# Kernel optimization log

Measured on AMD Instinct MI355X. Metric: run time of the kernel, lower is better.

## Reference

```python
import jax, jax.numpy as jnp
import numpy as np

N_NODES = 100000
N_EDGES = 1600000
IN_CH = 128
HEADS = 4
HID = 32
OUT_CH = 128
NEG_SLOPE = 0.2


def setup_inputs() -> dict:
    key = jax.random.key(0)
    ks = jax.random.split(key, 7)
    sc = 1.0 / np.sqrt(IN_CH)
    return {
        "x": jax.random.normal(ks[0], (N_NODES, IN_CH), dtype=jnp.float32),
        "edge_index": jax.random.randint(ks[1], (2, N_EDGES), 0, N_NODES, dtype=jnp.int32),
        "W": jax.random.normal(ks[2], (IN_CH, HEADS * HID), dtype=jnp.float32) * sc,
        "att_src": jax.random.normal(ks[3], (HEADS, HID), dtype=jnp.float32) * sc,
        "att_dst": jax.random.normal(ks[4], (HEADS, HID), dtype=jnp.float32) * sc,
        "lin_w": jax.random.normal(ks[5], (HEADS * HID, OUT_CH), dtype=jnp.float32) * (1.0 / np.sqrt(HEADS * HID)),
        "lin_b": jax.random.normal(ks[6], (OUT_CH,), dtype=jnp.float32) * 0.01,
    }


def reference(x, edge_index, W, att_src, att_dst, lin_w, lin_b):
    N = x.shape[0]
    src, dst = edge_index[0], edge_index[1]
    # node-wise linear transform -> [N, H, C]
    h = (x @ W).reshape(N, HEADS, HID)
    # per-node attention logit components [N, H]
    a_src = jnp.einsum("nhc,hc->nh", h, att_src)
    a_dst = jnp.einsum("nhc,hc->nh", h, att_dst)
    # per-edge logits with LeakyReLU [E, H]
    e = jax.nn.leaky_relu(a_src[src] + a_dst[dst], negative_slope=NEG_SLOPE)
    # segment softmax over destination neighborhoods
    m = jax.ops.segment_max(e, dst, num_segments=N)
    ex = jnp.exp(e - m[dst])
    s = jax.ops.segment_sum(ex, dst, num_segments=N)
    alpha = ex / (s[dst] + 1e-16)
    # weighted scatter-sum of source features [N, H, C] -> concat heads
    msg = h[src] * alpha[:, :, None]
    out = jax.ops.segment_sum(msg, dst, num_segments=N).reshape(N, HEADS * HID)
    # trailing dense + ReLU
    return jax.nn.relu(out @ lin_w + lin_b)
```

## Files before the change

### kernel.cpp

```cpp
#include <hip/hip_runtime.h>
#include <hip/hip_fp16.h>

#define NB   256
#define NBLK 128
#define BSH  9
#define DB   64
#define DBLK 128

typedef _Float16 f16;
typedef _Float16 half8 __attribute__((ext_vector_type(8)));
typedef __fp16 pk16x2 __attribute__((ext_vector_type(2)));
typedef float f32x4 __attribute__((ext_vector_type(4)));

__global__ void k_prep(const float* __restrict__ W, const float* __restrict__ LW,
                       f16* __restrict__ Wt, f16* __restrict__ LWt)
{
    int n = blockIdx.x & 127;
    const float* src = (blockIdx.x < 128) ? W : LW;
    f16* dst = (blockIdx.x < 128) ? Wt : LWt;
    int k = threadIdx.x;
    dst[n * 128 + k] = (f16)src[k * 128 + n];
}

__global__ __launch_bounds__(256) void k_gemm_att(
    const float* __restrict__ A, const f16* __restrict__ Wt,
    const float* __restrict__ att_s, const float* __restrict__ att_d,
    f16* __restrict__ Hh, float* __restrict__ as_out, float* __restrict__ ad_out,
    int M)
{
    __shared__ __align__(16) f16 as_lds[64 * 136];
    int t = threadIdx.x;
    int row0 = blockIdx.x * 64;

    {
        int r = t >> 2, kq = (t & 3) * 32;
        const float* ap = A + (size_t)(row0 + r) * 128 + kq;
        bool valid = (row0 + r) < M;
        pk16x2 hb[16];
#pragma unroll
        for (int j = 0; j < 8; ++j) {
            float4 v = valid ? *(const float4*)(ap + j * 4) : make_float4(0.f, 0.f, 0.f, 0.f);
            hb[2 * j]     = __builtin_amdgcn_cvt_pkrtz(v.x, v.y);
            hb[2 * j + 1] = __builtin_amdgcn_cvt_pkrtz(v.z, v.w);
        }
        f16* dst = as_lds + r * 136 + kq;
#pragma unroll
        for (int j = 0; j < 4; ++j) *(float4*)(dst + j * 8) = ((float4*)hb)[j];
    }
    __syncthreads();

    int w = t >> 6, ln = t & 63;
    int rr = (w & 1) * 32;
    int cc = (w >> 1) * 64;
    int q = ln >> 4, m = ln & 15;

    f32x4 acc[2][4];
#pragma unroll
    for (int i = 0; i < 2; ++i)
#pragma unroll
        for (int j = 0; j < 4; ++j) acc[i][j] = (f32x4){0.f, 0.f, 0.f, 0.f};

    const f16* wp = Wt + (size_t)(cc + m) * 128 + q * 8;
#pragma unroll
    for (int ks = 0; ks < 4; ++ks) {
        int k0 = ks * 32 + q * 8;
        half8 a0 = *(const half8*)(as_lds + (rr + m) * 136 + k0);
        half8 a1 = *(const half8*)(as_lds + (rr + 16 + m) * 136 + k0);
        half8 bf[4];
#pragma unroll
        for (int j = 0; j < 4; ++j)
            bf[j] = *(const half8*)(wp + j * 16 * 128 + ks * 32);
#pragma unroll
        for (int j = 0; j < 4; ++j) {
            acc[0][j] = __builtin_amdgcn_mfma_f32_16x16x32_f16(a0, bf[j], acc[0][j], 0, 0, 0);
            acc[1][j] = __builtin_amdgcn_mfma_f32_16x16x32_f16(a1, bf[j], acc[1][j], 0, 0, 0);
        }
    }
    __syncthreads();
#pragma unroll
    for (int i = 0; i < 2; ++i)
#pragma unroll
        for (int j = 0; j < 4; ++j)
#pragma unroll
            for (int g = 0; g < 4; ++g)
                as_lds[(rr + i * 16 + q * 4 + g) * 136 + cc + j * 16 + m] = (f16)acc[i][j][g];
    __syncthreads();
    {
        int r = t >> 2, cq = (t & 3) * 32;
        if (row0 + r < M) {
            float4 o0 = *(const float4*)(as_lds + r * 136 + cq);
            float4 o1 = *(const float4*)(as_lds + r * 136 + cq + 8);
            float4 o2 = *(const float4*)(as_lds + r * 136 + cq + 16);
            float4 o3 = *(const float4*)(as_lds + r * 136 + cq + 24);
            float4* hp = (float4*)(Hh + (size_t)(row0 + r) * 128 + cq);
            hp[0] = o0; hp[1] = o1; hp[2] = o2; hp[3] = o3;
        }
    }
    {
        int rl = w * 16 + m;
        int head = q;
        float ds = 0.f, dd = 0.f;
#pragma unroll
        for (int ch = 0; ch < 4; ++ch) {
            half8 hv = *(const half8*)(as_lds + rl * 136 + head * 32 + ch * 8);
            float4 s0 = *(const float4*)(att_s + head * 32 + ch * 8);
            float4 s1 = *(const float4*)(att_s + head * 32 + ch * 8 + 4);
            float4 d0 = *(const float4*)(att_d + head * 32 + ch * 8);
            float4 d1 = *(const float4*)(att_d + head * 32 + ch * 8 + 4);
            ds += (float)hv[0] * s0.x + (float)hv[1] * s0.y + (float)hv[2] * s0.z + (float)hv[3] * s0.w
                + (float)hv[4] * s1.x + (float)hv[5] * s1.y + (float)hv[6] * s1.z + (float)hv[7] * s1.w;
            dd += (float)hv[0] * d0.x + (float)hv[1] * d0.y + (float)hv[2] * d0.z + (float)hv[3] * d0.w
                + (float)hv[4] * d1.x + (float)hv[5] * d1.y + (float)hv[6] * d1.z + (float)hv[7] * d1.w;
        }
        if (row0 + rl < M) {
            as_out[(row0 + rl) * 4 + head] = ds;
            ad_out[(row0 + rl) * 4 + head] = dd;
        }
    }
}


__global__ __launch_bounds__(256) void k_ph_hist(
    const int* __restrict__ dst, int* __restrict__ bh, int E, int chunk)
{
    __shared__ int hist[NB];
    int t = threadIdx.x;
    hist[t] = 0;
    __syncthreads();
    int e0 = blockIdx.x * chunk;
    int e1 = min(e0 + chunk, E);
    for (int e = e0 + t; e < e1; e += 256)
        atomicAdd(&hist[dst[e] >> BSH], 1);
    __syncthreads();
    bh[t * NBLK + blockIdx.x] = hist[t];
}

__global__ __launch_bounds__(1024) void k_ph_scan(int* __restrict__ bh)
{
    __shared__ int sd[1024];
    const int per = (NB * NBLK) / 1024;
    int t = threadIdx.x;
    int base = t * per;
    int loc[per];
    int sum = 0;
#pragma unroll
    for (int j = 0; j < per; ++j) { loc[j] = bh[base + j]; sum += loc[j]; }
    sd[t] = sum;
    __syncthreads();
    for (int o = 1; o < 1024; o <<= 1) {
        int x = (t >= o) ? sd[t - o] : 0;
        __syncthreads();
        sd[t] += x;
        __syncthreads();
    }
    int run = sd[t] - sum;
#pragma unroll
    for (int j = 0; j < per; ++j) { bh[base + j] = run; run += loc[j]; }
}

__global__ __launch_bounds__(256) void k_ph_bin(
    const int* __restrict__ ei, const int* __restrict__ bh,
    int* __restrict__ binned, int E, int chunk)
{
    __shared__ int boff[NB];
    int t = threadIdx.x;
    boff[t] = bh[t * NBLK + blockIdx.x];
    __syncthreads();
    int e0 = blockIdx.x * chunk;
    int e1 = min(e0 + chunk, E);
    for (int e = e0 + t; e < e1; e += 256) {
        int s = ei[e];
        int d = ei[E + e];
        int p = atomicAdd(&boff[d >> BSH], 1);
        binned[p] = s | ((d & ((1 << BSH) - 1)) << 17);
    }
}

__global__ __launch_bounds__(256) void k_ph_csr(
    const int* __restrict__ binned, const int* __restrict__ bh,
    int* __restrict__ csr, int* __restrict__ off, int* __restrict__ deg,
    int N, int E)
{
    __shared__ int cnt[512], loff[512], sd[256];
    int b = blockIdx.x;
    int lo = b << BSH;
    if (lo >= N) return;
    int t = threadIdx.x;
    int seg = bh[b * NBLK];
    int segend = (b + 1 < NB) ? bh[(b + 1) * NBLK] : E;
    int len = segend - seg;
    cnt[t] = 0; cnt[t + 256] = 0;
    __syncthreads();
    for (int i = t; i < len; i += 256)
        atomicAdd(&cnt[(unsigned)binned[seg + i] >> 17], 1);
    __syncthreads();
    int a0 = cnt[2 * t], a1 = cnt[2 * t + 1];
    int s = a0 + a1;
    sd[t] = s;
    __syncthreads();
    for (int o = 1; o < 256; o <<= 1) {
        int x = (t >= o) ? sd[t - o] : 0;
        __syncthreads();
        sd[t] += x;
        __syncthreads();
    }
    int ex = sd[t] - s;
    loff[2 * t] = ex;
    loff[2 * t + 1] = ex + a0;
    int n0 = lo + 2 * t;
    if (n0 < N)     { off[n0] = seg + ex;          deg[n0] = a0; }
    if (n0 + 1 < N) { off[n0 + 1] = seg + ex + a0; deg[n0 + 1] = a1; }
    __syncthreads();
    for (int i = t; i < len; i += 256) {
        int v = binned[seg + i];
        int p = atomicAdd(&loff[(unsigned)v >> 17], 1);
        csr[seg + p] = v & 0x1ffff;
    }
}

__global__ __launch_bounds__(256) void k_dhist(
    const int* __restrict__ deg, int* __restrict__ dh, int N, int chunk)
{
    __shared__ int h[DB];
    int t = threadIdx.x;
    if (t < DB) h[t] = 0;
    __syncthreads();
    int e0 = blockIdx.x * chunk;
    int e1 = min(e0 + chunk, N);
    for (int i = e0 + t; i < e1; i += 256)
        atomicAdd(&h[min(deg[i], DB - 1)], 1);
    __syncthreads();
    if (t < DB) dh[t * DBLK + blockIdx.x] = h[t];
}

__global__ __launch_bounds__(1024) void k_dscan(int* __restrict__ dh)
{
    __shared__ int sd[1024];
    const int per = (DB * DBLK) / 1024;
    int t = threadIdx.x;
    int base = t * per;
    int loc[per];
    int sum = 0;
#pragma unroll
    for (int j = 0; j < per; ++j) { loc[j] = dh[base + j]; sum += loc[j]; }
    sd[t] = sum;
    __syncthreads();
    for (int o = 1; o < 1024; o <<= 1) {
        int x = (t >= o) ? sd[t - o] : 0;
        __syncthreads();
        sd[t] += x;
        __syncthreads();
    }
    int run = sd[t] - sum;
#pragma unroll
    for (int j = 0; j < per; ++j) { dh[base + j] = run; run += loc[j]; }
}

__global__ __launch_bounds__(256) void k_dscat(
    const int* __restrict__ deg, const int* __restrict__ dh,
    int* __restrict__ perm, int N, int chunk)
{
    __shared__ int boff[DB];
    int t = threadIdx.x;
    if (t < DB) boff[t] = dh[t * DBLK + blockIdx.x];
    __syncthreads();
    int e0 = blockIdx.x * chunk;
    int e1 = min(e0 + chunk, N);
    for (int i = e0 + t; i < e1; i += 256) {
        int p = atomicAdd(&boff[min(deg[i], DB - 1)], 1);
        perm[p] = i;
    }
}

__global__ __launch_bounds__(256) void k_gather_fused(
    const __half* __restrict__ Hh, const float* __restrict__ as_,
    const float* __restrict__ ad_, const int* __restrict__ off,
    const int* __restrict__ deg, const int* __restrict__ csr,
    const int* __restrict__ perm, const f16* __restrict__ LWt,
    const float* __restrict__ bias, float* __restrict__ Out, int N)
{
    __shared__ __align__(16) __half2 wh[16][68];
    __shared__ int srcs[16][16];
    __shared__ __align__(16) f16 pt[16][136];
    __shared__ int pnode[16];
    int t = threadIdx.x;
    int wid = t >> 6, lane = t & 63;
    int sub = lane >> 4;
    int li = lane & 15;
    int hh = li >> 2;
    int slot = wid * 4 + sub;
    int gbase = blockIdx.x * 16;
    if (t < 16) pnode[t] = (gbase + t < N) ? perm[gbase + t] : -1;
    __syncthreads();
    int n = pnode[slot];
    bool nvalid = n >= 0;
    int dg = nvalid ? deg[n] : 0;
    int base = nvalid ? off[n] : 0;
    float4 adn = nvalid ? *(const float4*)(ad_ + (size_t)n * 4)
                        : make_float4(0.f, 0.f, 0.f, 0.f);

    float s0 = 0.f, s1 = 0.f, s2 = 0.f, s3 = 0.f;
    float acc[8] = {0.f, 0.f, 0.f, 0.f, 0.f, 0.f, 0.f, 0.f};

    for (int c0 = 0; c0 < dg; c0 += 16) {
        int cnt = min(16, dg - c0);
        {
            int idx = c0 + li;
            int se = csr[base + min(idx, dg - 1)];
            float4 as = *(const float4*)(as_ + (size_t)se * 4);
            float e0 = as.x + adn.x, e1 = as.y + adn.y;
            float e2 = as.z + adn.z, e3 = as.w + adn.w;
            e0 = fmaxf(e0, 0.2f * e0); e1 = fmaxf(e1, 0.2f * e1);
            e2 = fmaxf(e2, 0.2f * e2); e3 = fmaxf(e3, 0.2f * e3);
            float x0 = __expf(e0), x1 = __expf(e1);
            float x2 = __expf(e2), x3 = __expf(e3);
            if (idx >= dg) { x0 = x1 = x2 = x3 = 0.f; }
            s0 += x0; s1 += x1; s2 += x2; s3 += x3;
            __half2 w4[4];
            w4[0] = __float2half2_rn(x0);
            w4[1] = __float2half2_rn(x1);
            w4[2] = __float2half2_rn(x2);
            w4[3] = __float2half2_rn(x3);
            *(float4*)&wh[slot][li * 4] = *(float4*)w4;
            srcs[slot][li] = se;
        }
        __asm__ volatile("s_waitcnt lgkmcnt(0)" ::: "memory");
        int quads = (cnt + 3) >> 2;
        __half2 ah[4];
        ah[0] = ah[1] = ah[2] = ah[3] = __float2half2_rn(0.f);
        for (int qq = 0; qq < quads; ++qq) {
#pragma unroll
            for (int u = 0; u < 4; ++u) {
                int i = qq * 4 + u;
                __half2 w2 = wh[slot][i * 4 + hh];
                int se = srcs[slot][i];
                float4 raw = *(const float4*)(Hh + (size_t)se * 128 + li * 8);
                __half2* ph = (__half2*)&raw;
                ah[0] = __hfma2(ph[0], w2, ah[0]);
                ah[1] = __hfma2(ph[1], w2, ah[1]);
                ah[2] = __hfma2(ph[2], w2, ah[2]);
                ah[3] = __hfma2(ph[3], w2, ah[3]);
            }
            if ((qq & 1) == 1) {
#pragma unroll
                for (int k = 0; k < 4; ++k) {
                    float2 f = __half22float2(ah[k]);
                    acc[2 * k] += f.x; acc[2 * k + 1] += f.y;
                    ah[k] = __float2half2_rn(0.f);
                }
            }
        }
#pragma unroll
        for (int k = 0; k < 4; ++k) {
            float2 f = __half22float2(ah[k]);
            acc[2 * k] += f.x; acc[2 * k + 1] += f.y;
        }
        __asm__ volatile("s_waitcnt lgkmcnt(0)" ::: "memory");
    }

#pragma unroll
    for (int o = 1; o < 16; o <<= 1) {
        s0 += __shfl_xor(s0, o);
        s1 += __shfl_xor(s1, o);
        s2 += __shfl_xor(s2, o);
        s3 += __shfl_xor(s3, o);
    }
    float sh = (hh == 0) ? s0 : (hh == 1) ? s1 : (hh == 2) ? s2 : s3;
    float inv = 1.f / (sh + 1e-16f);
    {
        __half2 o4[4];
#pragma unroll
        for (int k = 0; k < 4; ++k)
            o4[k] = __float22half2_rn(make_float2(acc[2 * k] * inv, acc[2 * k + 1] * inv));
        *(float4*)&pt[slot][li * 8] = *(float4*)o4;
    }
    __syncthreads();

    {
        int cc = wid * 32;
        f32x4 acc2[2];
        acc2[0] = (f32x4){0.f, 0.f, 0.f, 0.f};
        acc2[1] = (f32x4){0.f, 0.f, 0.f, 0.f};
        const f16* wp = LWt + (size_t)(cc + li) * 128 + sub * 8;
#pragma unroll
        for (int ks = 0; ks < 4; ++ks) {
            half8 a0 = *(const half8*)&pt[li][ks * 32 + sub * 8];
            half8 b0 = *(const half8*)(wp + ks * 32);
            half8 b1 = *(const half8*)(wp + 16 * 128 + ks * 32);
            acc2[0] = __builtin_amdgcn_mfma_f32_16x16x32_f16(a0, b0, acc2[0], 0, 0, 0);
            acc2[1] = __builtin_amdgcn_mfma_f32_16x16x32_f16(a0, b1, acc2[1], 0, 0, 0);
        }
        float bv0 = bias[cc + li];
        float bv1 = bias[cc + 16 + li];
#pragma unroll
        for (int g = 0; g < 4; ++g) {
            int r = sub * 4 + g;
            int node = pnode[r];
            if (node >= 0) {
                Out[(size_t)node * 128 + cc + li]      = fmaxf(acc2[0][g] + bv0, 0.f);
                Out[(size_t)node * 128 + cc + 16 + li] = fmaxf(acc2[1][g] + bv1, 0.f);
            }
        }
    }
}


extern "C" void kernel_launch(void* const* d_in, const int* in_sizes, int n_in,
                              void* d_out, int out_size, void* d_ws, size_t ws_size,
                              hipStream_t stream)
{
    const float* x     = (const float*)d_in[0];
    const int*   ei    = (const int*)d_in[1];
    const float* W     = (const float*)d_in[2];
    const float* att_s = (const float*)d_in[3];
    const float* att_d = (const float*)d_in[4];
    const float* lin_w = (const float*)d_in[5];
    const float* lin_b = (const float*)d_in[6];
    float* out = (float*)d_out;
    int N = in_sizes[0] / 128;
    int E = in_sizes[1] / 2;

    char* p = (char*)d_ws;
    auto alloc = [&](size_t bytes) { char* r = p; p += (bytes + 255) & ~(size_t)255; return r; };
    f16*    Hh   = (f16*)alloc((size_t)N * 128 * 2);
    f16*    Wt   = (f16*)alloc(128 * 128 * 2);
    f16*    LWt  = (f16*)alloc(128 * 128 * 2);
    float*  AS   = (float*)alloc((size_t)N * 4 * 4);
    float*  AD   = (float*)alloc((size_t)N * 4 * 4);
    int*    deg  = (int*)alloc((size_t)N * 4);
    int*    off  = (int*)alloc((size_t)N * 4);
    int*    perm = (int*)alloc((size_t)N * 4);
    int*    csr  = (int*)alloc((size_t)E * 4);
    int*    binned = (int*)alloc((size_t)E * 4);
    int*    bh   = (int*)alloc((size_t)NB * NBLK * 4);
    int*    dh   = (int*)alloc((size_t)DB * DBLK * 4);

    int chunk = (E + NBLK - 1) / NBLK;
    int nchunk = (N + DBLK - 1) / DBLK;
    int mb = (N + 63) / 64;
    k_prep<<<256, 128, 0, stream>>>(W, lin_w, Wt, LWt);
    k_gemm_att<<<mb, 256, 0, stream>>>(x, Wt, att_s, att_d, Hh, AS, AD, N);
    k_ph_hist<<<NBLK, 256, 0, stream>>>(ei + E, bh, E, chunk);
    k_ph_scan<<<1, 1024, 0, stream>>>(bh);
    k_ph_bin<<<NBLK, 256, 0, stream>>>(ei, bh, binned, E, chunk);
    k_ph_csr<<<NB, 256, 0, stream>>>(binned, bh, csr, off, deg, N, E);
    k_dhist<<<DBLK, 256, 0, stream>>>(deg, dh, N, nchunk);
    k_dscan<<<1, 1024, 0, stream>>>(dh);
    k_dscat<<<DBLK, 256, 0, stream>>>(deg, dh, perm, N, nchunk);
    k_gather_fused<<<(N + 15) / 16, 256, 0, stream>>>(
        (const __half*)Hh, AS, AD, off, deg, csr, perm, LWt, lin_b, out, N);
}
```

Baseline: 308.5 us.

## Drop degree-sorted node permutation and fuse weight prep with edge histogram

Removes the three-kernel degree bucketing pass (histogram, scan, scatter) that built a node permutation, so the fused gather kernel processes nodes in natural order. The weight transpose/convert kernel is merged with the destination histogram kernel into one launch. This cuts four kernel launches and their serialization. In exchange, gather blocks may get nodes of mixed degree, which can increase divergence inside a block.

```diff
diff --git a/kernel.cpp b/kernel.cpp
--- a/kernel.cpp
+++ b/kernel.cpp
@@ -4,22 +4,34 @@
 #define NB   256
 #define NBLK 128
 #define BSH  9
-#define DB   64
-#define DBLK 128
 
 typedef _Float16 f16;
 typedef _Float16 half8 __attribute__((ext_vector_type(8)));
 typedef __fp16 pk16x2 __attribute__((ext_vector_type(2)));
 typedef float f32x4 __attribute__((ext_vector_type(4)));
 
-__global__ void k_prep(const float* __restrict__ W, const float* __restrict__ LW,
-                       f16* __restrict__ Wt, f16* __restrict__ LWt)
-{
-    int n = blockIdx.x & 127;
-    const float* src = (blockIdx.x < 128) ? W : LW;
-    f16* dst = (blockIdx.x < 128) ? Wt : LWt;
-    int k = threadIdx.x;
-    dst[n * 128 + k] = (f16)src[k * 128 + n];
+__global__ __launch_bounds__(256) void k_setup(
+    const float* __restrict__ W, const float* __restrict__ LW,
+    f16* __restrict__ Wt, f16* __restrict__ LWt,
+    const int* __restrict__ dst, int* __restrict__ bh, int E, int chunk)
+{
+    int b = blockIdx.x;
+    int t = threadIdx.x;
+    if (b < 128) {
+        if (t < 128) Wt[b * 128 + t]  = (f16)W[t * 128 + b];
+        else         LWt[b * 128 + (t - 128)] = (f16)LW[(t - 128) * 128 + b];
+        return;
+    }
+    int blk = b - 128;
+    __shared__ int hist[NB];
+    hist[t] = 0;
+    __syncthreads();
+    int e0 = blk * chunk;
+    int e1 = min(e0 + chunk, E);
+    for (int e = e0 + t; e < e1; e += 256)
+        atomicAdd(&hist[dst[e] >> BSH], 1);
+    __syncthreads();
+    bh[t * NBLK + blk] = hist[t];
 }
 
 __global__ __launch_bounds__(256) void k_gemm_att(
@@ -120,21 +132,6 @@
 }
 
 
-__global__ __launch_bounds__(256) void k_ph_hist(
-    const int* __restrict__ dst, int* __restrict__ bh, int E, int chunk)
-{
-    __shared__ int hist[NB];
-    int t = threadIdx.x;
-    hist[t] = 0;
-    __syncthreads();
-    int e0 = blockIdx.x * chunk;
-    int e1 = min(e0 + chunk, E);
-    for (int e = e0 + t; e < e1; e += 256)
-        atomicAdd(&hist[dst[e] >> BSH], 1);
-    __syncthreads();
-    bh[t * NBLK + blockIdx.x] = hist[t];
-}
-
 __global__ __launch_bounds__(1024) void k_ph_scan(int* __restrict__ bh)
 {
     __shared__ int sd[1024];
@@ -218,71 +215,16 @@
     }
 }
 
-__global__ __launch_bounds__(256) void k_dhist(
-    const int* __restrict__ deg, int* __restrict__ dh, int N, int chunk)
-{
-    __shared__ int h[DB];
-    int t = threadIdx.x;
-    if (t < DB) h[t] = 0;
-    __syncthreads();
-    int e0 = blockIdx.x * chunk;
-    int e1 = min(e0 + chunk, N);
-    for (int i = e0 + t; i < e1; i += 256)
-        atomicAdd(&h[min(deg[i], DB - 1)], 1);
-    __syncthreads();
-    if (t < DB) dh[t * DBLK + blockIdx.x] = h[t];
-}
-
-__global__ __launch_bounds__(1024) void k_dscan(int* __restrict__ dh)
-{
-    __shared__ int sd[1024];
-    const int per = (DB * DBLK) / 1024;
-    int t = threadIdx.x;
-    int base = t * per;
-    int loc[per];
-    int sum = 0;
-#pragma unroll
-    for (int j = 0; j < per; ++j) { loc[j] = dh[base + j]; sum += loc[j]; }
-    sd[t] = sum;
-    __syncthreads();
-    for (int o = 1; o < 1024; o <<= 1) {
-        int x = (t >= o) ? sd[t - o] : 0;
-        __syncthreads();
-        sd[t] += x;
-        __syncthreads();
-    }
-    int run = sd[t] - sum;
-#pragma unroll
-    for (int j = 0; j < per; ++j) { dh[base + j] = run; run += loc[j]; }
-}
-
-__global__ __launch_bounds__(256) void k_dscat(
-    const int* __restrict__ deg, const int* __restrict__ dh,
-    int* __restrict__ perm, int N, int chunk)
-{
-    __shared__ int boff[DB];
-    int t = threadIdx.x;
-    if (t < DB) boff[t] = dh[t * DBLK + blockIdx.x];
-    __syncthreads();
-    int e0 = blockIdx.x * chunk;
-    int e1 = min(e0 + chunk, N);
-    for (int i = e0 + t; i < e1; i += 256) {
-        int p = atomicAdd(&boff[min(deg[i], DB - 1)], 1);
-        perm[p] = i;
-    }
-}
-
 __global__ __launch_bounds__(256) void k_gather_fused(
     const __half* __restrict__ Hh, const float* __restrict__ as_,
     const float* __restrict__ ad_, const int* __restrict__ off,
     const int* __restrict__ deg, const int* __restrict__ csr,
-    const int* __restrict__ perm, const f16* __restrict__ LWt,
-    const float* __restrict__ bias, float* __restrict__ Out, int N)
+    const f16* __restrict__ LWt, const float* __restrict__ bias,
+    float* __restrict__ Out, int N)
 {
     __shared__ __align__(16) __half2 wh[16][68];
     __shared__ int srcs[16][16];
     __shared__ __align__(16) f16 pt[16][136];
-    __shared__ int pnode[16];
     int t = threadIdx.x;
     int wid = t >> 6, lane = t & 63;
     int sub = lane >> 4;
@@ -290,10 +232,8 @@
     int hh = li >> 2;
     int slot = wid * 4 + sub;
     int gbase = blockIdx.x * 16;
-    if (t < 16) pnode[t] = (gbase + t < N) ? perm[gbase + t] : -1;
-    __syncthreads();
-    int n = pnode[slot];
-    bool nvalid = n >= 0;
+    int n = gbase + slot;
+    bool nvalid = n < N;
     int dg = nvalid ? deg[n] : 0;
     int base = nvalid ? off[n] : 0;
     float4 adn = nvalid ? *(const float4*)(ad_ + (size_t)n * 4)
@@ -395,8 +335,8 @@
 #pragma unroll
         for (int g = 0; g < 4; ++g) {
             int r = sub * 4 + g;
-            int node = pnode[r];
-            if (node >= 0) {
+            int node = gbase + r;
+            if (node < N) {
                 Out[(size_t)node * 128 + cc + li]      = fmaxf(acc2[0][g] + bv0, 0.f);
                 Out[(size_t)node * 128 + cc + 16 + li] = fmaxf(acc2[1][g] + bv1, 0.f);
             }
@@ -429,24 +369,17 @@
     float*  AD   = (float*)alloc((size_t)N * 4 * 4);
     int*    deg  = (int*)alloc((size_t)N * 4);
     int*    off  = (int*)alloc((size_t)N * 4);
-    int*    perm = (int*)alloc((size_t)N * 4);
     int*    csr  = (int*)alloc((size_t)E * 4);
     int*    binned = (int*)alloc((size_t)E * 4);
     int*    bh   = (int*)alloc((size_t)NB * NBLK * 4);
-    int*    dh   = (int*)alloc((size_t)DB * DBLK * 4);
 
     int chunk = (E + NBLK - 1) / NBLK;
-    int nchunk = (N + DBLK - 1) / DBLK;
     int mb = (N + 63) / 64;
-    k_prep<<<256, 128, 0, stream>>>(W, lin_w, Wt, LWt);
+    k_setup<<<256, 256, 0, stream>>>(W, lin_w, Wt, LWt, ei + E, bh, E, chunk);
     k_gemm_att<<<mb, 256, 0, stream>>>(x, Wt, att_s, att_d, Hh, AS, AD, N);
-    k_ph_hist<<<NBLK, 256, 0, stream>>>(ei + E, bh, E, chunk);
     k_ph_scan<<<1, 1024, 0, stream>>>(bh);
     k_ph_bin<<<NBLK, 256, 0, stream>>>(ei, bh, binned, E, chunk);
     k_ph_csr<<<NB, 256, 0, stream>>>(binned, bh, csr, off, deg, N, E);
-    k_dhist<<<DBLK, 256, 0, stream>>>(deg, dh, N, nchunk);
-    k_dscan<<<1, 1024, 0, stream>>>(dh);
-    k_dscat<<<DBLK, 256, 0, stream>>>(deg, dh, perm, N, nchunk);
     k_gather_fused<<<(N + 15) / 16, 256, 0, stream>>>(
-        (const __half*)Hh, AS, AD, off, deg, csr, perm, LWt, lin_b, out, N);
-}
+        (const __half*)Hh, AS, AD, off, deg, csr, LWt, lin_b, out, N);
+}
```

Measured after the change: 289.2 us. -6.2%, faster.
